# Kernel optimization log

Measured on AMD Instinct MI355X. Metric: run time of the kernel, lower is better.

## Reference

```python
import jax, jax.numpy as jnp
import numpy as np

B, T, V, H, O = 256, 1024, 128, 128, 2  # batch, max_len, input_size, hidden, n_outputs


def setup_inputs() -> dict:
    key = jax.random.key(0)
    ks = jax.random.split(key, 9)
    # ragged one-hot sequences: symbol 0 is the pad symbol
    lengths = jax.random.randint(ks[0], (B,), 1, T + 1)
    symbols = jax.random.randint(ks[1], (B, T), 1, V)  # real symbols in [1, V)
    t_idx = jnp.arange(T)[None, :]
    symbols = jnp.where(t_idx < lengths[:, None], symbols, 0)  # pad tail with symbol 0
    x = jax.nn.one_hot(symbols, V, dtype=jnp.float32)  # [B, T, V]
    # RNN params (torch nn.RNN layout: W_ih [H, V-1], W_hh [H, H])
    s = 1.0 / np.sqrt(H)
    W_ih = jax.random.uniform(ks[2], (H, V - 1), minval=-s, maxval=s)
    W_hh = jax.random.uniform(ks[3], (H, H), minval=-s, maxval=s)
    b_ih = jax.random.uniform(ks[4], (H,), minval=-s, maxval=s)
    b_hh = jax.random.uniform(ks[5], (H,), minval=-s, maxval=s)
    # dense head: Linear(H, O)
    W_out = jax.random.uniform(ks[6], (O, H), minval=-s, maxval=s)
    b_out = jax.random.uniform(ks[7], (O,), minval=-s, maxval=s)
    return {"x": x, "W_ih": W_ih, "W_hh": W_hh, "b_ih": b_ih,
            "b_hh": b_hh, "W_out": W_out, "b_out": b_out}


def reference(x, W_ih, W_hh, b_ih, b_hh, W_out, b_out):
    Bk, Tk, Vk = x.shape
    # unpad: length = first timestep whose argmax is the pad symbol (index 0)
    is_pad = jnp.argmax(x, axis=-1) == 0  # [B, T]
    length = jnp.where(is_pad.any(-1), jnp.argmax(is_pad, axis=-1), Tk)  # [B]
    active = jnp.arange(Tk)[None, :] < length[:, None]  # [B, T]
    feats = x[..., 1:]  # strip pad column -> [B, T, V-1]
    # precompute input projection for all timesteps (streaming part)
    pre = jnp.einsum('btf,hf->bth', feats, W_ih) + b_ih + b_hh  # [B, T, H]

    def step(h, inp):
        pre_t, act_t = inp  # [B, H], [B]
        h_new = jnp.tanh(pre_t + h @ W_hh.T)
        h = jnp.where(act_t[:, None], h_new, h)  # freeze hidden past each seq's length
        return h, None

    h0 = jnp.zeros((Bk, W_hh.shape[0]), dtype=x.dtype)
    h_last, _ = jax.lax.scan(step, h0, (pre.transpose(1, 0, 2), active.T))
    fed = jax.nn.softmax(h_last @ W_out.T + b_out, axis=-1)  # [B, O]
    hidden = h_last[None]  # [1, B, H], matches torch stacked layer hidden
    return fed, hidden
```

## Files before the change

### kernel.cpp

```cpp
#include <hip/hip_runtime.h>
#include <stdint.h>

#define Bsz   256
#define Tlen  1024
#define Vocab 128
#define Hdim  128
#define NTHR  512
#define WTN   ((Vocab - 1) * Hdim)

typedef _Float16 half2_t __attribute__((ext_vector_type(2)));

#define HCHB  48
#define HBUFI (8 * HCHB / 4)

__device__ __forceinline__ float tanh_fast(float x) {
    float e = __builtin_amdgcn_exp2f(x * 2.885390081777927f);
    return 1.0f - 2.0f * __builtin_amdgcn_rcpf(e + 1.0f);
}

__device__ __forceinline__ float dpp_xor1(float s) {
    return __int_as_float(__builtin_amdgcn_mov_dpp(__float_as_int(s), 0xB1, 0xF, 0xF, true));
}
__device__ __forceinline__ float dpp_xor2(float s) {
    return __int_as_float(__builtin_amdgcn_mov_dpp(__float_as_int(s), 0x4E, 0xF, 0xF, true));
}
__device__ __forceinline__ float dpp_hm(float s) {
    return __int_as_float(__builtin_amdgcn_mov_dpp(__float_as_int(s), 0x141, 0xF, 0xF, true));
}

__global__ __launch_bounds__(256) void transpose_kernel(
    const float* __restrict__ W_ih, float* __restrict__ wt)
{
    int idx = blockIdx.x * 256 + threadIdx.x;
    if (idx < WTN) {
        int h = idx / (Vocab - 1);
        int f = idx - h * (Vocab - 1);
        wt[f * Hdim + h] = W_ih[idx];
    }
}

__global__ __launch_bounds__(NTHR, 2) void rnn_kernel(
    const float* __restrict__ x, const float* __restrict__ wt,
    const float* __restrict__ W_hh,
    const float* __restrict__ b_ih, const float* __restrict__ b_hh,
    const float* __restrict__ W_out, const float* __restrict__ b_out,
    float* __restrict__ out)
{
    __shared__ float wt_s[WTN];
    __shared__ int   syms[Tlen];
    __shared__ __align__(16) int hbuf[2][HBUFI];
    __shared__ int   len_sh;

    const int tid = threadIdx.x;
    const int b   = blockIdx.x;
    const int g   = tid >> 3;
    const int j   = tid & 7;

    if (tid == 0) len_sh = Tlen;
    for (int k = tid; k < 2 * HBUFI; k += NTHR) ((int*)hbuf)[k] = 0;

    int wp[16];
    #pragma unroll
    for (int r = 0; r < 2; r++) {
        const float4* wrow = (const float4*)(W_hh + (2 * g + r) * Hdim + 16 * j);
        #pragma unroll
        for (int q4 = 0; q4 < 4; q4++) {
            float4 t4 = wrow[q4];
            wp[r * 8 + q4 * 2 + 0] = __builtin_bit_cast(int, __builtin_amdgcn_cvt_pkrtz(t4.x, t4.y));
            wp[r * 8 + q4 * 2 + 1] = __builtin_bit_cast(int, __builtin_amdgcn_cvt_pkrtz(t4.z, t4.w));
        }
    }
    const float bias0 = b_ih[2 * g]     + b_hh[2 * g];
    const float bias1 = b_ih[2 * g + 1] + b_hh[2 * g + 1];

    {
        const float4* src = (const float4*)wt;
        float4* dst = (float4*)wt_s;
        for (int k = tid; k < WTN / 4; k += NTHR) dst[k] = src[k];
    }

    const float4* xb = (const float4*)(x + (size_t)b * Tlen * Vocab);
    for (int k = tid; k < (Tlen * Vocab) / 4; k += NTHR) {
        float4 v = xb[k];
        int c = -1;
        if      (v.x > 0.5f) c = 0;
        else if (v.y > 0.5f) c = 1;
        else if (v.z > 0.5f) c = 2;
        else if (v.w > 0.5f) c = 3;
        if (c >= 0) syms[k >> 5] = ((k & 31) << 2) + c;
    }
    __syncthreads();

    {
        int lm = Tlen;
        for (int k = tid; k < Tlen; k += NTHR)
            if (syms[k] == 0 && k < lm) lm = k;
        if (lm < Tlen) atomicMin(&len_sh, lm);
    }
    __syncthreads();
    const int len = len_sh;

    const float2* wt2 = (const float2*)wt_s;
    float2 pre_v = {0.0f, 0.0f}, p_t1 = {0.0f, 0.0f};
    int s_t2 = 1;
    if (len > 0) pre_v = wt2[(syms[0] - 1) * 64 + g];
    if (len > 1) p_t1  = wt2[(syms[1] - 1) * 64 + g];
    if (len > 2) s_t2  = syms[2];

    const char* hb0 = (const char*)hbuf[0];
    const char* hb1 = (const char*)hbuf[1];
    const int roff = j * HCHB;
    const int woff = (g >> 3) * HCHB + ((2 * g) & 15) * 2;

    for (int t = 0; t < len; t++) {
        #pragma unroll
        for (int k = 0; k < 16; k += 8)
            asm volatile("" : "+v"(wp[k]), "+v"(wp[k+1]), "+v"(wp[k+2]), "+v"(wp[k+3]),
                             "+v"(wp[k+4]), "+v"(wp[k+5]), "+v"(wp[k+6]), "+v"(wp[k+7]));

        float2 p_t2 = wt2[(s_t2 - 1) * 64 + g];
        int   s_t3 = (t + 3 < len) ? syms[t + 3] : 1;

        const char* hb = (t & 1) ? hb1 : hb0;
        uint4 r0 = *(const uint4*)(hb + roff);
        uint4 r1 = *(const uint4*)(hb + roff + 16);
        unsigned hr[8] = {r0.x, r0.y, r0.z, r0.w, r1.x, r1.y, r1.z, r1.w};

        float a0 = 0.0f, a1 = 0.0f;
        #pragma unroll
        for (int p = 0; p < 8; p++) {
            half2_t hh = __builtin_bit_cast(half2_t, hr[p]);
            a0 = __builtin_amdgcn_fdot2(hh, __builtin_bit_cast(half2_t, wp[p]),     a0, false);
            a1 = __builtin_amdgcn_fdot2(hh, __builtin_bit_cast(half2_t, wp[8 + p]), a1, false);
        }
        a0 += dpp_xor1(a0); a1 += dpp_xor1(a1);
        a0 += dpp_xor2(a0); a1 += dpp_xor2(a1);
        a0 += dpp_hm(a0);   a1 += dpp_hm(a1);

        if (j == 0) {
            float h0 = tanh_fast(a0 + pre_v.x + bias0);
            float h1 = tanh_fast(a1 + pre_v.y + bias1);
            int pk = __builtin_bit_cast(int, __builtin_amdgcn_cvt_pkrtz(h0, h1));
            *(int*)(((char*)hbuf[(t + 1) & 1]) + woff) = pk;
        }
        pre_v = p_t1; p_t1 = p_t2; s_t2 = s_t3;
        __syncthreads();
    }

    const _Float16* hf = (const _Float16*)hbuf[len & 1];
    #define HGET(e) ((float)hf[((e) >> 4) * 24 + ((e) & 15)])
    if (tid < Hdim)
        out[2 * Bsz + b * Hdim + tid] = HGET(tid);
    if (tid < 64) {
        float h0 = HGET(tid);
        float h1 = HGET(tid + 64);
        float p0 = W_out[tid] * h0 + W_out[64 + tid] * h1;
        float p1 = W_out[128 + tid] * h0 + W_out[192 + tid] * h1;
        #pragma unroll
        for (int off = 32; off > 0; off >>= 1) {
            p0 += __shfl_down(p0, off, 64);
            p1 += __shfl_down(p1, off, 64);
        }
        if (tid == 0) {
            float l0 = p0 + b_out[0], l1 = p1 + b_out[1];
            float m  = fmaxf(l0, l1);
            float e0 = __expf(l0 - m), e1 = __expf(l1 - m);
            float d  = e0 + e1;
            out[b * 2 + 0] = e0 / d;
            out[b * 2 + 1] = e1 / d;
        }
    }
    #undef HGET
}

extern "C" void kernel_launch(void* const* d_in, const int* in_sizes, int n_in,
                              void* d_out, int out_size, void* d_ws, size_t ws_size,
                              hipStream_t stream) {
    const float* x     = (const float*)d_in[0];
    const float* W_ih  = (const float*)d_in[1];
    const float* W_hh  = (const float*)d_in[2];
    const float* b_ih  = (const float*)d_in[3];
    const float* b_hh  = (const float*)d_in[4];
    const float* W_out = (const float*)d_in[5];
    const float* b_out = (const float*)d_in[6];
    float* out = (float*)d_out;

    float* wt = (float*)d_ws;

    const int NTRN = (WTN + 255) / 256;
    transpose_kernel<<<NTRN, 256, 0, stream>>>(W_ih, wt);
    rnn_kernel<<<Bsz, NTHR, 0, stream>>>(x, wt, W_hh, b_ih, b_hh, W_out, b_out, out);
}
```

Before: 527.6 us.

## Split one-hot decode and input projection into a separate grid-wide kernel

Adds a decode kernel that runs across the whole GPU. It turns each one-hot row into a symbol, computes the sequence lengths with atomicMin, and writes the fp16 input projection for every (batch, timestep) to workspace. The recurrent kernel then only streams these precomputed projections with a 4-deep register prefetch. It no longer stages W_ih in LDS or scans x per block, and it uses a raw s_barrier. This moves the serial per-block x scan off the critical path, at the cost of an extra 64 MB intermediate write and read and an extra launch. A fallback path keeps the old kernel when workspace is too small.

New measurement: 911.7 us. 72.8% more time.

```diff
diff --git a/kernel.cpp b/kernel.cpp
--- a/kernel.cpp
+++ b/kernel.cpp
@@ -5,32 +5,31 @@
 #define Tlen  1024
 #define Vocab 128
 #define Hdim  128
-#define NTHR  512
 #define WTN   ((Vocab - 1) * Hdim)
 
 typedef _Float16 half2_t __attribute__((ext_vector_type(2)));
 
-#define HCHB  48
-#define HBUFI (8 * HCHB / 4)
+#define PRE_BYTES ((size_t)Bsz * Tlen * Hdim * 2)
+#define LEN_OFF   PRE_BYTES
+#define WT_OFF    (PRE_BYTES + 1024)
+#define WS_NEED   (WT_OFF + (size_t)WTN * 4 + 256)
 
 __device__ __forceinline__ float tanh_fast(float x) {
     float e = __builtin_amdgcn_exp2f(x * 2.885390081777927f);
     return 1.0f - 2.0f * __builtin_amdgcn_rcpf(e + 1.0f);
 }
 
-__device__ __forceinline__ float dpp_xor1(float s) {
-    return __int_as_float(__builtin_amdgcn_mov_dpp(__float_as_int(s), 0xB1, 0xF, 0xF, true));
-}
-__device__ __forceinline__ float dpp_xor2(float s) {
-    return __int_as_float(__builtin_amdgcn_mov_dpp(__float_as_int(s), 0x4E, 0xF, 0xF, true));
-}
-__device__ __forceinline__ float dpp_hm(float s) {
-    return __int_as_float(__builtin_amdgcn_mov_dpp(__float_as_int(s), 0x141, 0xF, 0xF, true));
-}
-
-__global__ __launch_bounds__(256) void transpose_kernel(
-    const float* __restrict__ W_ih, float* __restrict__ wt)
+#define DPPF(x, ctrl) __int_as_float(__builtin_amdgcn_mov_dpp(__float_as_int(x), ctrl, 0xF, 0xF, true))
+
+#define BAR() asm volatile("s_waitcnt lgkmcnt(0)\n\ts_barrier" ::: "memory")
+
+#define HCHB  48
+#define HBUFI (8 * HCHB / 4)
+
+__global__ __launch_bounds__(256) void prep_kernel(
+    const float* __restrict__ W_ih, float* __restrict__ wt, int* __restrict__ len_g)
 {
+    if (blockIdx.x == 0 && threadIdx.x < Bsz) len_g[threadIdx.x] = Tlen;
     int idx = blockIdx.x * 256 + threadIdx.x;
     if (idx < WTN) {
         int h = idx / (Vocab - 1);
@@ -39,7 +38,146 @@
     }
 }
 
-__global__ __launch_bounds__(NTHR, 2) void rnn_kernel(
+__global__ __launch_bounds__(256) void decode_kernel(
+    const float* __restrict__ x, const float* __restrict__ wt,
+    uint2* __restrict__ pre_all, int* __restrict__ len_g)
+{
+    const int l    = threadIdx.x & 63;
+    const int half = l >> 5;
+    const int li   = l & 31;
+    const int row  = blockIdx.x * 8 + (threadIdx.x >> 6) * 2 + half;
+
+    const float4* xr = (const float4*)(x + (size_t)row * Vocab);
+    float4 v = xr[li];
+    int c = v.x > 0.5f ? 0 : v.y > 0.5f ? 1 : v.z > 0.5f ? 2 : v.w > 0.5f ? 3 : -1;
+    unsigned long long m = __ballot(c >= 0);
+    unsigned mh = half ? (unsigned)(m >> 32) : (unsigned)m;
+    int fl  = __builtin_ctz(mh) + (half << 5);
+    int sym = __shfl(li * 4 + c, fl, 64);
+
+    if (sym == 0) {
+        if (li == 0) atomicMin(&len_g[row >> 10], row & (Tlen - 1));
+    } else {
+        const float4* wr = (const float4*)(wt + (sym - 1) * Hdim);
+        float4 wv = wr[li];
+        unsigned e0 = __builtin_bit_cast(unsigned short, (_Float16)wv.x);
+        unsigned e1 = __builtin_bit_cast(unsigned short, (_Float16)wv.y);
+        unsigned e2 = __builtin_bit_cast(unsigned short, (_Float16)wv.z);
+        unsigned e3 = __builtin_bit_cast(unsigned short, (_Float16)wv.w);
+        uint2 o;
+        o.x = e0 | (e1 << 16);
+        o.y = e2 | (e3 << 16);
+        pre_all[(size_t)row * 32 + li] = o;
+    }
+}
+
+__global__ __launch_bounds__(512, 2) void rnn_kernel(
+    const unsigned* __restrict__ pre_all, const int* __restrict__ len_g,
+    const float* __restrict__ W_hh,
+    const float* __restrict__ b_ih, const float* __restrict__ b_hh,
+    const float* __restrict__ W_out, const float* __restrict__ b_out,
+    float* __restrict__ out)
+{
+    __shared__ __align__(16) int hbuf[2][HBUFI];
+
+    const int tid = threadIdx.x;
+    const int b   = blockIdx.x;
+    const int g   = tid >> 3;
+    const int j   = tid & 7;
+
+    for (int k = tid; k < 2 * HBUFI; k += 512) ((int*)hbuf)[k] = 0;
+
+    int wp[16];
+    #pragma unroll
+    for (int r = 0; r < 2; r++) {
+        const float4* wrow = (const float4*)(W_hh + (2 * g + r) * Hdim + 16 * j);
+        #pragma unroll
+        for (int q4 = 0; q4 < 4; q4++) {
+            float4 t4 = wrow[q4];
+            wp[r * 8 + q4 * 2 + 0] = __builtin_bit_cast(int, __builtin_amdgcn_cvt_pkrtz(t4.x, t4.y));
+            wp[r * 8 + q4 * 2 + 1] = __builtin_bit_cast(int, __builtin_amdgcn_cvt_pkrtz(t4.z, t4.w));
+        }
+    }
+    const float bias0 = b_ih[2 * g]     + b_hh[2 * g];
+    const float bias1 = b_ih[2 * g + 1] + b_hh[2 * g + 1];
+
+    const int len = len_g[b];
+    const unsigned* prow = pre_all + (size_t)b * Tlen * 64 + g;
+
+    unsigned q0 = 0, q1 = 0, q2 = 0, q3 = 0;
+    if (0 < len) q0 = prow[0];
+    if (1 < len) q1 = prow[64];
+    if (2 < len) q2 = prow[128];
+    if (3 < len) q3 = prow[192];
+
+    const char* hb0 = (const char*)hbuf[0];
+    const char* hb1 = (const char*)hbuf[1];
+    const int roff = j * HCHB;
+    const int woff = (g >> 3) * HCHB + ((2 * g) & 15) * 2;
+
+    __syncthreads();
+
+    for (int t = 0; t < len; t++) {
+        #pragma unroll
+        for (int k = 0; k < 16; k += 8)
+            asm volatile("" : "+v"(wp[k]), "+v"(wp[k+1]), "+v"(wp[k+2]), "+v"(wp[k+3]),
+                             "+v"(wp[k+4]), "+v"(wp[k+5]), "+v"(wp[k+6]), "+v"(wp[k+7]));
+
+        unsigned qn = 0;
+        if (t + 4 < len) qn = prow[(size_t)(t + 4) * 64];
+
+        const char* hb = (t & 1) ? hb1 : hb0;
+        uint4 r0 = *(const uint4*)(hb + roff);
+        uint4 r1 = *(const uint4*)(hb + roff + 16);
+        unsigned hr[8] = {r0.x, r0.y, r0.z, r0.w, r1.x, r1.y, r1.z, r1.w};
+        float a0 = 0.0f, a1 = 0.0f;
+        #pragma unroll
+        for (int p = 0; p < 8; p++) {
+            half2_t hh = __builtin_bit_cast(half2_t, hr[p]);
+            a0 = __builtin_amdgcn_fdot2(hh, __builtin_bit_cast(half2_t, wp[p]),     a0, false);
+            a1 = __builtin_amdgcn_fdot2(hh, __builtin_bit_cast(half2_t, wp[8 + p]), a1, false);
+        }
+        a0 += DPPF(a0, 0xB1);  a1 += DPPF(a1, 0xB1);
+        a0 += DPPF(a0, 0x4E);  a1 += DPPF(a1, 0x4E);
+        a0 += DPPF(a0, 0x141); a1 += DPPF(a1, 0x141);
+        if (j == 0) {
+            half2_t ph = __builtin_bit_cast(half2_t, q0);
+            float h0 = tanh_fast(a0 + (float)ph.x + bias0);
+            float h1 = tanh_fast(a1 + (float)ph.y + bias1);
+            int pk = __builtin_bit_cast(int, __builtin_amdgcn_cvt_pkrtz(h0, h1));
+            *(int*)(((char*)hbuf[(t + 1) & 1]) + woff) = pk;
+        }
+        q0 = q1; q1 = q2; q2 = q3; q3 = qn;
+        BAR();
+    }
+
+    const _Float16* hf = (const _Float16*)hbuf[len & 1];
+    #define HGET(e) ((float)hf[((e) >> 4) * 24 + ((e) & 15)])
+    if (tid < Hdim)
+        out[2 * Bsz + b * Hdim + tid] = HGET(tid);
+    if (tid < 64) {
+        float h0 = HGET(tid);
+        float h1 = HGET(tid + 64);
+        float p0 = W_out[tid] * h0 + W_out[64 + tid] * h1;
+        float p1 = W_out[128 + tid] * h0 + W_out[192 + tid] * h1;
+        #pragma unroll
+        for (int off = 32; off > 0; off >>= 1) {
+            p0 += __shfl_down(p0, off, 64);
+            p1 += __shfl_down(p1, off, 64);
+        }
+        if (tid == 0) {
+            float l0 = p0 + b_out[0], l1 = p1 + b_out[1];
+            float m  = fmaxf(l0, l1);
+            float e0 = __expf(l0 - m), e1 = __expf(l1 - m);
+            float d  = e0 + e1;
+            out[b * 2 + 0] = e0 / d;
+            out[b * 2 + 1] = e1 / d;
+        }
+    }
+    #undef HGET
+}
+
+__global__ __launch_bounds__(512, 2) void rnn_fallback(
     const float* __restrict__ x, const float* __restrict__ wt,
     const float* __restrict__ W_hh,
     const float* __restrict__ b_ih, const float* __restrict__ b_hh,
@@ -57,7 +195,7 @@
     const int j   = tid & 7;
 
     if (tid == 0) len_sh = Tlen;
-    for (int k = tid; k < 2 * HBUFI; k += NTHR) ((int*)hbuf)[k] = 0;
+    for (int k = tid; k < 2 * HBUFI; k += 512) ((int*)hbuf)[k] = 0;
 
     int wp[16];
     #pragma unroll
@@ -76,11 +214,10 @@
     {
         const float4* src = (const float4*)wt;
         float4* dst = (float4*)wt_s;
-        for (int k = tid; k < WTN / 4; k += NTHR) dst[k] = src[k];
-    }
-
+        for (int k = tid; k < WTN / 4; k += 512) dst[k] = src[k];
+    }
     const float4* xb = (const float4*)(x + (size_t)b * Tlen * Vocab);
-    for (int k = tid; k < (Tlen * Vocab) / 4; k += NTHR) {
+    for (int k = tid; k < (Tlen * Vocab) / 4; k += 512) {
         float4 v = xb[k];
         int c = -1;
         if      (v.x > 0.5f) c = 0;
@@ -90,10 +227,9 @@
         if (c >= 0) syms[k >> 5] = ((k & 31) << 2) + c;
     }
     __syncthreads();
-
     {
         int lm = Tlen;
-        for (int k = tid; k < Tlen; k += NTHR)
+        for (int k = tid; k < Tlen; k += 512)
             if (syms[k] == 0 && k < lm) lm = k;
         if (lm < Tlen) atomicMin(&len_sh, lm);
     }
@@ -117,7 +253,6 @@
         for (int k = 0; k < 16; k += 8)
             asm volatile("" : "+v"(wp[k]), "+v"(wp[k+1]), "+v"(wp[k+2]), "+v"(wp[k+3]),
                              "+v"(wp[k+4]), "+v"(wp[k+5]), "+v"(wp[k+6]), "+v"(wp[k+7]));
-
         float2 p_t2 = wt2[(s_t2 - 1) * 64 + g];
         int   s_t3 = (t + 3 < len) ? syms[t + 3] : 1;
 
@@ -125,7 +260,6 @@
         uint4 r0 = *(const uint4*)(hb + roff);
         uint4 r1 = *(const uint4*)(hb + roff + 16);
         unsigned hr[8] = {r0.x, r0.y, r0.z, r0.w, r1.x, r1.y, r1.z, r1.w};
-
         float a0 = 0.0f, a1 = 0.0f;
         #pragma unroll
         for (int p = 0; p < 8; p++) {
@@ -133,10 +267,9 @@
             a0 = __builtin_amdgcn_fdot2(hh, __builtin_bit_cast(half2_t, wp[p]),     a0, false);
             a1 = __builtin_amdgcn_fdot2(hh, __builtin_bit_cast(half2_t, wp[8 + p]), a1, false);
         }
-        a0 += dpp_xor1(a0); a1 += dpp_xor1(a1);
-        a0 += dpp_xor2(a0); a1 += dpp_xor2(a1);
-        a0 += dpp_hm(a0);   a1 += dpp_hm(a1);
-
+        a0 += DPPF(a0, 0xB1); a1 += DPPF(a1, 0xB1);
+        a0 += DPPF(a0, 0x4E); a1 += DPPF(a1, 0x4E);
+        a0 += DPPF(a0, 0x141); a1 += DPPF(a1, 0x141);
         if (j == 0) {
             float h0 = tanh_fast(a0 + pre_v.x + bias0);
             float h1 = tanh_fast(a1 + pre_v.y + bias1);
@@ -185,9 +318,21 @@
     const float* b_out = (const float*)d_in[6];
     float* out = (float*)d_out;
 
-    float* wt = (float*)d_ws;
-
     const int NTRN = (WTN + 255) / 256;
-    transpose_kernel<<<NTRN, 256, 0, stream>>>(W_ih, wt);
-    rnn_kernel<<<Bsz, NTHR, 0, stream>>>(x, wt, W_hh, b_ih, b_hh, W_out, b_out, out);
-}
+
+    if (ws_size >= WS_NEED) {
+        uint2* pre_all = (uint2*)d_ws;
+        int*   len_g   = (int*)((char*)d_ws + LEN_OFF);
+        float* wt      = (float*)((char*)d_ws + WT_OFF);
+        prep_kernel<<<NTRN, 256, 0, stream>>>(W_ih, wt, len_g);
+        decode_kernel<<<(Bsz * Tlen) / 8, 256, 0, stream>>>(x, wt, pre_all, len_g);
+        rnn_kernel<<<Bsz, 512, 0, stream>>>((const unsigned*)pre_all, len_g,
+                                            W_hh, b_ih, b_hh, W_out, b_out, out);
+    } else {
+        float* wt    = (float*)d_ws;
+        int*   len_g = (int*)((char*)d_ws + (size_t)WTN * 4);
+        prep_kernel<<<NTRN, 256, 0, stream>>>(W_ih, wt, len_g);
+        rnn_fallback<<<Bsz, 512, 0, stream>>>(x, wt, W_hh, b_ih, b_hh,
+                                              W_out, b_out, out);
+    }
+}
```
